# Kernel tuning notes

Measured on AMD Instinct MI355X. Metric: run time of the kernel, lower is better.

Reference implementation:

```python
import jax, jax.numpy as jnp
import numpy as np

H_BANDWIDTH = 0.5
EPS = 1e-5


def setup_inputs() -> dict:
    key = jax.random.key(0)
    k1, k2 = jax.random.split(key)
    x = jax.random.normal(k1, (4, 256, 64, 64), dtype=jnp.float32)
    y = jax.random.normal(k2, (4, 256, 64, 64), dtype=jnp.float32)
    return {"x": x, "y": y}


def reference(x, y):
    # x, y: (N, C, H, W), H=W=64 so no pooling branch is taken
    N, C, H, W = x.shape
    # mean over batch and spatial dims of y -> per-channel mu, shape (1, C, 1, 1)
    y_mu = jnp.mean(y, axis=(0, 2, 3)).reshape(1, C, 1, 1)
    x_c = x - y_mu
    y_c = y - y_mu
    # L2-normalize over channel dim
    x_n = x_c / jnp.linalg.norm(x_c, axis=1, keepdims=True)
    y_n = y_c / jnp.linalg.norm(y_c, axis=1, keepdims=True)
    x_n = x_n.reshape(N, C, H * W)
    y_n = y_n.reshape(N, C, H * W)
    # cosine similarity: (N, HW, HW)
    cos = jnp.einsum("ncp,ncq->npq", x_n, y_n)
    d = 1.0 - cos
    d_min = jnp.min(d, axis=2, keepdims=True)
    d_tilde = d / (d_min + EPS)
    w = jnp.exp((1.0 - d_tilde) / H_BANDWIDTH)
    cx_ij = w / jnp.sum(w, axis=2, keepdims=True)
    cx = jnp.mean(jnp.max(cx_ij, axis=1), axis=1)  # (N,)
    cx_loss = jnp.mean(-jnp.log(cx + EPS))
    return cx_loss
```

## Files before the change

kernel.cpp:

```cpp
#include <hip/hip_runtime.h>
#include <hip/hip_bf16.h>

typedef short bf16x8 __attribute__((ext_vector_type(8)));
typedef float f32x4 __attribute__((ext_vector_type(4)));

#define NB 4
#define C 256
#define HW 4096
#define NROWS (NB * HW)
#define EPSF 1e-5f

__device__ __forceinline__ unsigned short f2bf(float f) {
    unsigned int u = __float_as_uint(f);
    unsigned int r = u + 0x7fffu + ((u >> 16) & 1u);
    return (unsigned short)(r >> 16);
}
__device__ __forceinline__ float bf2f(unsigned int h) {
    return __uint_as_float(h << 16);
}
__device__ __forceinline__ void unpack8(uint4 u, float* v) {
    unsigned int w0 = u.x, w1 = u.y, w2 = u.z, w3 = u.w;
    v[0] = bf2f(w0 & 0xffffu); v[1] = bf2f(w0 >> 16);
    v[2] = bf2f(w1 & 0xffffu); v[3] = bf2f(w1 >> 16);
    v[4] = bf2f(w2 & 0xffffu); v[5] = bf2f(w2 >> 16);
    v[6] = bf2f(w3 & 0xffffu); v[7] = bf2f(w3 >> 16);
}
__device__ __forceinline__ float waveReduceSum(float v) {
    for (int off = 32; off > 0; off >>= 1) v += __shfl_xor(v, off);
    return v;
}
typedef __attribute__((address_space(1))) const unsigned int glb_cu;
typedef __attribute__((address_space(3))) unsigned int lds_u;
__device__ __forceinline__ void async_copy16(const unsigned short* g, unsigned short* l) {
    __builtin_amdgcn_global_load_lds((glb_cu*)g, (lds_u*)l, 16, 0, 0);
}

__global__ __launch_bounds__(256) void mu_kernel(const float* __restrict__ y,
                                                 float* __restrict__ mu) {
    int c = blockIdx.x;
    int tid = threadIdx.x;
    float s = 0.f;
    const float* base = y + (size_t)c * HW;
    for (int n = 0; n < NB; n++) {
        const float* bn = base + (size_t)n * C * HW;
        for (int i = tid; i < HW; i += 256) s += bn[i];
    }
    s = waveReduceSum(s);
    __shared__ float red[4];
    int lane = tid & 63, wave = tid >> 6;
    if (lane == 0) red[wave] = s;
    __syncthreads();
    if (tid == 0) mu[c] = (red[0] + red[1] + red[2] + red[3]) * (1.0f / 16384.0f);
}

#define TP 32
#define TSTRIDE 257
__global__ __launch_bounds__(256) void prep_kernel(const float* __restrict__ x,
                                                   const float* __restrict__ y,
                                                   const float* __restrict__ mu,
                                                   unsigned short* __restrict__ Xn,
                                                   unsigned short* __restrict__ Yn) {
    __shared__ float smu[C];
    __shared__ float tile[TP * TSTRIDE];
    __shared__ float red[8 * 32];
    __shared__ float invn[TP];
    int tid = threadIdx.x;
    smu[tid] = mu[tid];
    int blk = blockIdx.x;
    int n = blk >> 7;
    int p0 = (blk & 127) * TP;
    int tp = tid & 31, cc = tid >> 5;
    __syncthreads();
    for (int pass = 0; pass < 2; pass++) {
        const float* in = pass ? y : x;
        unsigned short* out = pass ? Yn : Xn;
        const float* base = in + (size_t)n * C * HW + p0 + tp;
        float ssq = 0.f;
        for (int c = cc; c < C; c += 8) {
            float v = base[(size_t)c * HW] - smu[c];
            tile[tp * TSTRIDE + c] = v;
            ssq += v * v;
        }
        red[cc * 32 + tp] = ssq;
        __syncthreads();
        if (tid < 32) {
            float s = 0.f;
            for (int k = 0; k < 8; k++) s += red[k * 32 + tid];
            invn[tid] = rsqrtf(s);
        }
        __syncthreads();
        int c2 = (tid & 127) * 2;
        int pp = tid >> 7;
        for (int p = pp; p < TP; p += 2) {
            float inv = invn[p];
            unsigned short b0 = f2bf(tile[p * TSTRIDE + c2] * inv);
            unsigned short b1 = f2bf(tile[p * TSTRIDE + c2 + 1] * inv);
            unsigned int pack = (unsigned int)b0 | ((unsigned int)b1 << 16);
            ((unsigned int*)out)[(size_t)(n * HW + p0 + p) * (C / 2) + (c2 >> 1)] = pack;
        }
        __syncthreads();
    }
}

#define EPSTRIDE 136
__global__ __launch_bounds__(256, 2) void gemm_cos(const unsigned short* __restrict__ Xn,
                                                   const unsigned short* __restrict__ Yn,
                                                   unsigned short* __restrict__ Cos) {
    __shared__ unsigned short lds_us[32768];
    int n = blockIdx.z;
    int pBase = blockIdx.y * 128, qBase = blockIdx.x * 128;
    const unsigned short* Ab = Xn + ((size_t)n * HW + pBase) * C;
    const unsigned short* Bb = Yn + ((size_t)n * HW + qBase) * C;
    int tid = threadIdx.x, lane = tid & 63, wave = tid >> 6;
    int wm = (wave >> 1) * 64, wn = (wave & 1) * 64;
    int mrow = lane & 15, quad = lane >> 4;

    f32x4 acc[4][4];
#pragma unroll
    for (int i = 0; i < 4; i++)
#pragma unroll
        for (int j = 0; j < 4; j++) acc[i][j] = (f32x4){0.f, 0.f, 0.f, 0.f};

#pragma unroll
    for (int h = 0; h < 2; h++) {
#pragma unroll
        for (int mat = 0; mat < 2; mat++) {
            const unsigned short* g = mat ? Bb : Ab;
            unsigned short* lbase = lds_us + mat * 16384;
#pragma unroll
            for (int t = 0; t < 8; t++) {
                int slot = t * 256 + tid;
                int r = slot >> 4, cl = slot & 15;
                int c = h * 16 + (cl ^ (r & 15));
                async_copy16(g + (size_t)r * C + c * 8, lbase + slot * 8);
            }
        }
        __syncthreads();
#pragma unroll
        for (int kkl = 0; kkl < 4; kkl++) {
            int cl4 = kkl * 4 + quad;
            int clp = cl4 ^ mrow;
            bf16x8 af[4], bfr[4];
#pragma unroll
            for (int i = 0; i < 4; i++) {
                af[i]  = *(const bf16x8*)(lds_us + (wm + i * 16 + mrow) * 128 + clp * 8);
                bfr[i] = *(const bf16x8*)(lds_us + 16384 + (wn + i * 16 + mrow) * 128 + clp * 8);
            }
#pragma unroll
            for (int i = 0; i < 4; i++)
#pragma unroll
                for (int j = 0; j < 4; j++)
                    acc[i][j] = __builtin_amdgcn_mfma_f32_16x16x32_bf16(af[i], bfr[j], acc[i][j], 0, 0, 0);
        }
        __syncthreads();
    }

    unsigned short* epb = lds_us;
    int col = lane & 15, quad4 = quad * 4;
#pragma unroll
    for (int i = 0; i < 4; i++)
#pragma unroll
        for (int j = 0; j < 4; j++)
#pragma unroll
            for (int r = 0; r < 4; r++)
                epb[(wm + i * 16 + quad4 + r) * EPSTRIDE + wn + j * 16 + col] = f2bf(acc[i][j][r]);
    __syncthreads();
    unsigned short* Crow = Cos + (size_t)n * HW * HW;
#pragma unroll
    for (int it = 0; it < 8; it++) {
        int e = it * 2048 + tid * 8;
        int r = e >> 7, cg = e & 127;
        uint4 o = *(const uint4*)(epb + r * EPSTRIDE + cg);
        *(uint4*)(Crow + (size_t)(pBase + r) * HW + qBase + cg) = o;
    }
}

__global__ __launch_bounds__(256, 3) void rowcol(const unsigned short* __restrict__ Cos,
                                                 unsigned short* __restrict__ partial) {
    int n = blockIdx.y, chunk = blockIdx.x;
    int tid = threadIdx.x, lane = tid & 63, wave = tid >> 6;
    const unsigned short* rowbase = Cos + ((size_t)n * HW + chunk * 8) * HW;
    __shared__ float redm[8][4];
    __shared__ float sval[8][4];

    uint4 d[8][2];
#pragma unroll
    for (int r = 0; r < 8; r++) {
        const unsigned short* rp = rowbase + (size_t)r * HW;
        d[r][0] = *(const uint4*)(rp + tid * 8);
        d[r][1] = *(const uint4*)(rp + 2048 + tid * 8);
    }

    float m8[8];
#pragma unroll
    for (int r = 0; r < 8; r++) {
        float v[16];
        unpack8(d[r][0], v); unpack8(d[r][1], v + 8);
        float m = v[0];
#pragma unroll
        for (int k = 1; k < 16; k++) m = fmaxf(m, v[k]);
        m8[r] = m;
    }
#pragma unroll
    for (int off = 32; off > 0; off >>= 1)
#pragma unroll
        for (int r = 0; r < 8; r++) m8[r] = fmaxf(m8[r], __shfl_xor(m8[r], off));
    if (lane == 0)
#pragma unroll
        for (int r = 0; r < 8; r++) redm[r][wave] = m8[r];
    __syncthreads();

    float alpha[8], basec[8];
#pragma unroll
    for (int r = 0; r < 8; r++) {
        float M = fmaxf(fmaxf(redm[r][0], redm[r][1]), fmaxf(redm[r][2], redm[r][3]));
        alpha[r] = 2.0f / ((1.0f - M) + EPSF);
        basec[r] = 2.0f - alpha[r];
    }

    float s8[8];
#pragma unroll
    for (int r = 0; r < 8; r++) {
        float v[16];
        unpack8(d[r][0], v); unpack8(d[r][1], v + 8);
        float s = 0.f;
#pragma unroll
        for (int k = 0; k < 16; k++) s += __expf(fmaf(alpha[r], v[k], basec[r]));
        s8[r] = s;
    }
#pragma unroll
    for (int off = 32; off > 0; off >>= 1)
#pragma unroll
        for (int r = 0; r < 8; r++) s8[r] += __shfl_xor(s8[r], off);
    if (lane == 0)
#pragma unroll
        for (int r = 0; r < 8; r++) sval[r][wave] = s8[r];
    __syncthreads();

    float cmax[16];
#pragma unroll
    for (int k = 0; k < 16; k++) cmax[k] = -1e30f;
#pragma unroll
    for (int r = 0; r < 8; r++) {
        float S = sval[r][0] + sval[r][1] + sval[r][2] + sval[r][3];
        float beta = basec[r] - __logf(S);
        float v[16];
        unpack8(d[r][0], v); unpack8(d[r][1], v + 8);
#pragma unroll
        for (int k = 0; k < 16; k++) cmax[k] = fmaxf(cmax[k], fmaf(alpha[r], v[k], beta));
    }

    unsigned short* outp = partial + ((size_t)(n * 512 + chunk)) * HW;
    uint4 o0, o1;
    o0.x = (unsigned int)f2bf(cmax[0]) | ((unsigned int)f2bf(cmax[1]) << 16);
    o0.y = (unsigned int)f2bf(cmax[2]) | ((unsigned int)f2bf(cmax[3]) << 16);
    o0.z = (unsigned int)f2bf(cmax[4]) | ((unsigned int)f2bf(cmax[5]) << 16);
    o0.w = (unsigned int)f2bf(cmax[6]) | ((unsigned int)f2bf(cmax[7]) << 16);
    o1.x = (unsigned int)f2bf(cmax[8]) | ((unsigned int)f2bf(cmax[9]) << 16);
    o1.y = (unsigned int)f2bf(cmax[10]) | ((unsigned int)f2bf(cmax[11]) << 16);
    o1.z = (unsigned int)f2bf(cmax[12]) | ((unsigned int)f2bf(cmax[13]) << 16);
    o1.w = (unsigned int)f2bf(cmax[14]) | ((unsigned int)f2bf(cmax[15]) << 16);
    *(uint4*)(outp + tid * 8) = o0;
    *(uint4*)(outp + 2048 + tid * 8) = o1;
}

__global__ __launch_bounds__(256) void colmax1(const unsigned short* __restrict__ partial,
                                               float* __restrict__ partial2) {
    int n = blockIdx.z, cg = blockIdx.y;
    int q0 = blockIdx.x * 2048 + threadIdx.x * 8;
    const unsigned short* p = partial + ((size_t)(n * 512 + cg * 32)) * HW + q0;
    float mx[8];
#pragma unroll
    for (int k = 0; k < 8; k++) mx[k] = -1e30f;
    for (int c = 0; c < 32; c++) {
        uint4 u = *(const uint4*)(p + (size_t)c * HW);
        float v[8];
        unpack8(u, v);
#pragma unroll
        for (int k = 0; k < 8; k++) mx[k] = fmaxf(mx[k], v[k]);
    }
    float* o = partial2 + ((size_t)(n * 16 + cg)) * HW + q0;
#pragma unroll
    for (int k = 0; k < 8; k += 4) {
        float4 ov = {mx[k], mx[k + 1], mx[k + 2], mx[k + 3]};
        *(float4*)(o + k) = ov;
    }
}

__global__ __launch_bounds__(1024) void colfinal2(const float* __restrict__ partial2,
                                                  float* __restrict__ cxsum) {
    int n = blockIdx.x;
    int tid = threadIdx.x;
    const float* p = partial2 + (size_t)n * 16 * HW + tid * 4;
    float4 m = {-1e30f, -1e30f, -1e30f, -1e30f};
#pragma unroll
    for (int g = 0; g < 16; g++) {
        float4 v = *(const float4*)(p + (size_t)g * HW);
        m.x = fmaxf(m.x, v.x); m.y = fmaxf(m.y, v.y);
        m.z = fmaxf(m.z, v.z); m.w = fmaxf(m.w, v.w);
    }
    float s = __expf(m.x) + __expf(m.y) + __expf(m.z) + __expf(m.w);
    s = waveReduceSum(s);
    __shared__ float red[16];
    int lane = tid & 63, wave = tid >> 6;
    if (lane == 0) red[wave] = s;
    __syncthreads();
    if (tid == 0) {
        float S = 0.f;
        for (int w = 0; w < 16; w++) S += red[w];
        cxsum[n] = S;
    }
}

__global__ void finalize(const float* __restrict__ cxsum, float* __restrict__ out) {
    if (threadIdx.x == 0 && blockIdx.x == 0) {
        float loss = 0.f;
        for (int n = 0; n < NB; n++) {
            float cx = cxsum[n] * (1.0f / 4096.0f);
            loss += -logf(cx + EPSF);
        }
        out[0] = loss * 0.25f;
    }
}

extern "C" void kernel_launch(void* const* d_in, const int* in_sizes, int n_in,
                              void* d_out, int out_size, void* d_ws, size_t ws_size,
                              hipStream_t stream) {
    const float* x = (const float*)d_in[0];
    const float* y = (const float*)d_in[1];
    float* out = (float*)d_out;
    char* ws = (char*)d_ws;

    float* mu               = (float*)(ws + 0);
    float* cxsum            = (float*)(ws + 1024);
    float* partial2         = (float*)(ws + 65536);
    unsigned short* Xn      = (unsigned short*)(ws + 2097152);
    unsigned short* Yn      = (unsigned short*)(ws + 10485760);
    unsigned short* partial = (unsigned short*)(ws + 2097152);
    unsigned short* Cos     = (unsigned short*)(ws + 18874368);

    mu_kernel<<<C, 256, 0, stream>>>(y, mu);
    prep_kernel<<<NROWS / TP, 256, 0, stream>>>(x, y, mu, Xn, Yn);
    gemm_cos<<<dim3(HW / 128, HW / 128, NB), 256, 0, stream>>>(Xn, Yn, Cos);
    rowcol<<<dim3(512, NB), 256, 0, stream>>>(Cos, partial);
    colmax1<<<dim3(2, 16, NB), 256, 0, stream>>>(partial, partial2);
    colfinal2<<<NB, 1024, 0, stream>>>(partial2, cxsum);
    finalize<<<1, 64, 0, stream>>>(cxsum, out);
}
```

Measured before the change: 199.3 us.

## Fuse row-max into GEMM epilogue and halve GEMM LDS footprint

```diff
diff --git a/kernel.cpp b/kernel.cpp
--- a/kernel.cpp
+++ b/kernel.cpp
@@ -103,12 +103,14 @@
 }
 
 #define EPSTRIDE 136
-__global__ __launch_bounds__(256, 2) void gemm_cos(const unsigned short* __restrict__ Xn,
+__global__ __launch_bounds__(256, 3) void gemm_cos(const unsigned short* __restrict__ Xn,
                                                    const unsigned short* __restrict__ Yn,
-                                                   unsigned short* __restrict__ Cos) {
-    __shared__ unsigned short lds_us[32768];
+                                                   unsigned short* __restrict__ Cos,
+                                                   float* __restrict__ rowmaxp) {
+    __shared__ unsigned short lds_us[16384];
     int n = blockIdx.z;
-    int pBase = blockIdx.y * 128, qBase = blockIdx.x * 128;
+    int qb = blockIdx.x;
+    int pBase = blockIdx.y * 128, qBase = qb * 128;
     const unsigned short* Ab = Xn + ((size_t)n * HW + pBase) * C;
     const unsigned short* Bb = Yn + ((size_t)n * HW + qBase) * C;
     int tid = threadIdx.x, lane = tid & 63, wave = tid >> 6;
@@ -122,29 +124,30 @@
         for (int j = 0; j < 4; j++) acc[i][j] = (f32x4){0.f, 0.f, 0.f, 0.f};
 
 #pragma unroll
-    for (int h = 0; h < 2; h++) {
+    for (int st = 0; st < 4; st++) {
 #pragma unroll
         for (int mat = 0; mat < 2; mat++) {
             const unsigned short* g = mat ? Bb : Ab;
-            unsigned short* lbase = lds_us + mat * 16384;
-#pragma unroll
-            for (int t = 0; t < 8; t++) {
+            unsigned short* lbase = lds_us + mat * 8192;
+#pragma unroll
+            for (int t = 0; t < 4; t++) {
                 int slot = t * 256 + tid;
-                int r = slot >> 4, cl = slot & 15;
-                int c = h * 16 + (cl ^ (r & 15));
+                int r = slot >> 3, cl = slot & 7;
+                int c = st * 8 + (cl ^ (r & 7));
                 async_copy16(g + (size_t)r * C + c * 8, lbase + slot * 8);
             }
         }
         __syncthreads();
 #pragma unroll
-        for (int kkl = 0; kkl < 4; kkl++) {
-            int cl4 = kkl * 4 + quad;
-            int clp = cl4 ^ mrow;
+        for (int kk = 0; kk < 2; kk++) {
+            int lc = kk * 4 + quad;
             bf16x8 af[4], bfr[4];
 #pragma unroll
             for (int i = 0; i < 4; i++) {
-                af[i]  = *(const bf16x8*)(lds_us + (wm + i * 16 + mrow) * 128 + clp * 8);
-                bfr[i] = *(const bf16x8*)(lds_us + 16384 + (wn + i * 16 + mrow) * 128 + clp * 8);
+                int ra = wm + i * 16 + mrow;
+                af[i] = *(const bf16x8*)(lds_us + (ra * 8 + (lc ^ (ra & 7))) * 8);
+                int rb = wn + i * 16 + mrow;
+                bfr[i] = *(const bf16x8*)(lds_us + 8192 + (rb * 8 + (lc ^ (rb & 7))) * 8);
             }
 #pragma unroll
             for (int i = 0; i < 4; i++)
@@ -157,30 +160,59 @@
 
     unsigned short* epb = lds_us;
     int col = lane & 15, quad4 = quad * 4;
-#pragma unroll
-    for (int i = 0; i < 4; i++)
-#pragma unroll
-        for (int j = 0; j < 4; j++)
-#pragma unroll
-            for (int r = 0; r < 4; r++)
-                epb[(wm + i * 16 + quad4 + r) * EPSTRIDE + wn + j * 16 + col] = f2bf(acc[i][j][r]);
-    __syncthreads();
     unsigned short* Crow = Cos + (size_t)n * HW * HW;
 #pragma unroll
-    for (int it = 0; it < 8; it++) {
-        int e = it * 2048 + tid * 8;
-        int r = e >> 7, cg = e & 127;
-        uint4 o = *(const uint4*)(epb + r * EPSTRIDE + cg);
-        *(uint4*)(Crow + (size_t)(pBase + r) * HW + qBase + cg) = o;
-    }
+    for (int half = 0; half < 2; half++) {
+        if (wm == half * 64) {
+#pragma unroll
+            for (int i = 0; i < 4; i++)
+#pragma unroll
+                for (int j = 0; j < 4; j++)
+#pragma unroll
+                    for (int r = 0; r < 4; r++)
+                        epb[(i * 16 + quad4 + r) * EPSTRIDE + wn + j * 16 + col] = f2bf(acc[i][j][r]);
+        }
+        __syncthreads();
+#pragma unroll
+        for (int it = 0; it < 4; it++) {
+            int e = it * 2048 + tid * 8;
+            int r = e >> 7, cg = e & 127;
+            uint4 o = *(const uint4*)(epb + r * EPSTRIDE + cg);
+            *(uint4*)(Crow + (size_t)(pBase + half * 64 + r) * HW + qBase + cg) = o;
+            float v[8];
+            unpack8(o, v);
+            float m = fmaxf(fmaxf(fmaxf(v[0], v[1]), fmaxf(v[2], v[3])),
+                            fmaxf(fmaxf(v[4], v[5]), fmaxf(v[6], v[7])));
+            m = fmaxf(m, __shfl_xor(m, 1));
+            m = fmaxf(m, __shfl_xor(m, 2));
+            m = fmaxf(m, __shfl_xor(m, 4));
+            m = fmaxf(m, __shfl_xor(m, 8));
+            if ((tid & 15) == 0)
+                rowmaxp[(size_t)qb * NROWS + n * HW + pBase + half * 64 + r] = m;
+        }
+        if (half == 0) __syncthreads();
+    }
+}
+
+__global__ __launch_bounds__(256) void rowred(const float* __restrict__ rowmaxp,
+                                              float* __restrict__ alphaArr,
+                                              float* __restrict__ baseArr) {
+    int idx = blockIdx.x * 256 + threadIdx.x;
+    float m = -1e30f;
+#pragma unroll
+    for (int qb = 0; qb < 32; qb++) m = fmaxf(m, rowmaxp[(size_t)qb * NROWS + idx]);
+    float a = 2.0f / ((1.0f - m) + EPSF);
+    alphaArr[idx] = a;
+    baseArr[idx] = 2.0f - a;
 }
 
 __global__ __launch_bounds__(256, 3) void rowcol(const unsigned short* __restrict__ Cos,
+                                                 const float* __restrict__ alphaArr,
+                                                 const float* __restrict__ baseArr,
                                                  unsigned short* __restrict__ partial) {
     int n = blockIdx.y, chunk = blockIdx.x;
     int tid = threadIdx.x, lane = tid & 63, wave = tid >> 6;
     const unsigned short* rowbase = Cos + ((size_t)n * HW + chunk * 8) * HW;
-    __shared__ float redm[8][4];
     __shared__ float sval[8][4];
 
     uint4 d[8][2];
@@ -190,32 +222,12 @@
         d[r][0] = *(const uint4*)(rp + tid * 8);
         d[r][1] = *(const uint4*)(rp + 2048 + tid * 8);
     }
-
-    float m8[8];
+    int row0 = n * HW + chunk * 8;
+    float alpha[8], basec[8];
 #pragma unroll
     for (int r = 0; r < 8; r++) {
-        float v[16];
-        unpack8(d[r][0], v); unpack8(d[r][1], v + 8);
-        float m = v[0];
-#pragma unroll
-        for (int k = 1; k < 16; k++) m = fmaxf(m, v[k]);
-        m8[r] = m;
-    }
-#pragma unroll
-    for (int off = 32; off > 0; off >>= 1)
-#pragma unroll
-        for (int r = 0; r < 8; r++) m8[r] = fmaxf(m8[r], __shfl_xor(m8[r], off));
-    if (lane == 0)
-#pragma unroll
-        for (int r = 0; r < 8; r++) redm[r][wave] = m8[r];
-    __syncthreads();
-
-    float alpha[8], basec[8];
-#pragma unroll
-    for (int r = 0; r < 8; r++) {
-        float M = fmaxf(fmaxf(redm[r][0], redm[r][1]), fmaxf(redm[r][2], redm[r][3]));
-        alpha[r] = 2.0f / ((1.0f - M) + EPSF);
-        basec[r] = 2.0f - alpha[r];
+        alpha[r] = alphaArr[row0 + r];
+        basec[r] = baseArr[row0 + r];
     }
 
     float s8[8];
@@ -333,16 +345,20 @@
 
     float* mu               = (float*)(ws + 0);
     float* cxsum            = (float*)(ws + 1024);
-    float* partial2         = (float*)(ws + 65536);
-    unsigned short* Xn      = (unsigned short*)(ws + 2097152);
-    unsigned short* Yn      = (unsigned short*)(ws + 10485760);
-    unsigned short* partial = (unsigned short*)(ws + 2097152);
-    unsigned short* Cos     = (unsigned short*)(ws + 18874368);
+    float* alphaArr         = (float*)(ws + 65536);
+    float* baseArr          = (float*)(ws + 131072);
+    float* partial2         = (float*)(ws + 262144);
+    float* rowmaxp          = (float*)(ws + 1310720);
+    unsigned short* Xn      = (unsigned short*)(ws + 4194304);
+    unsigned short* Yn      = (unsigned short*)(ws + 12582912);
+    unsigned short* partial = (unsigned short*)(ws + 4194304);
+    unsigned short* Cos     = (unsigned short*)(ws + 20971520);
 
     mu_kernel<<<C, 256, 0, stream>>>(y, mu);
     prep_kernel<<<NROWS / TP, 256, 0, stream>>>(x, y, mu, Xn, Yn);
-    gemm_cos<<<dim3(HW / 128, HW / 128, NB), 256, 0, stream>>>(Xn, Yn, Cos);
-    rowcol<<<dim3(512, NB), 256, 0, stream>>>(Cos, partial);
+    gemm_cos<<<dim3(HW / 128, HW / 128, NB), 256, 0, stream>>>(Xn, Yn, Cos, rowmaxp);
+    rowred<<<NROWS / 256, 256, 0, stream>>>(rowmaxp, alphaArr, baseArr);
+    rowcol<<<dim3(512, NB), 256, 0, stream>>>(Cos, alphaArr, baseArr, partial);
     colmax1<<<dim3(2, 16, NB), 256, 0, stream>>>(partial, partial2);
     colfinal2<<<NB, 1024, 0, stream>>>(partial2, cxsum);
     finalize<<<1, 64, 0, stream>>>(cxsum, out);
```

Result: slower. 211.6 us (+6.2%).
